# Performance work log

Measured on AMD Instinct MI355X. Metric: run time of the kernel, lower is better.

The kernel has to match this reference:

```python
import jax, jax.numpy as jnp
import numpy as np

N_NODES = 100000
N_EDGES = 1600000
F_IN = 128
HID = 64
HORIZON = 100
NUM_TARGETS = 3


def setup_inputs() -> dict:
    key = jax.random.key(0)
    ks = jax.random.split(key, 7)
    x = jax.random.normal(ks[0], (N_NODES, F_IN), dtype=jnp.float32)
    edge_index = jax.random.randint(ks[1], (2, N_EDGES), 0, N_NODES, dtype=jnp.int64)
    s = 1.0 / np.sqrt(F_IN)
    W_l = jax.random.uniform(ks[2], (HID, F_IN), jnp.float32, -s, s)
    b_l = jax.random.uniform(ks[3], (HID,), jnp.float32, -s, s)
    W_r = jax.random.uniform(ks[4], (HID, F_IN), jnp.float32, -s, s)
    s2 = 1.0 / np.sqrt(HID)
    W_out = jax.random.uniform(ks[5], (NUM_TARGETS * HORIZON, HID), jnp.float32, -s2, s2)
    b_out = jax.random.uniform(ks[6], (NUM_TARGETS * HORIZON,), jnp.float32, -s2, s2)
    return {"x": x, "edge_index": edge_index, "W_l": W_l, "b_l": b_l,
            "W_r": W_r, "W_out": W_out, "b_out": b_out}


def reference(x, edge_index, W_l, b_l, W_r, W_out, b_out):
    n = x.shape[0]
    src, dst = edge_index[0], edge_index[1]
    # gather neighbor features and mean-aggregate per destination node
    msgs = x[src]  # [E, F_IN]
    agg = jax.ops.segment_sum(msgs, dst, num_segments=n)  # [N, F_IN]
    cnt = jax.ops.segment_sum(jnp.ones((edge_index.shape[1],), x.dtype), dst, num_segments=n)
    mean = agg / jnp.maximum(cnt, 1.0)[:, None]
    # SAGEConv: lin_l(aggregated) + lin_r(root), bias only on lin_l
    h = jnp.einsum('nf,hf->nh', mean, W_l) + b_l + jnp.einsum('nf,hf->nh', x, W_r)
    h = jax.nn.relu(h)
    out = jnp.einsum('nh,oh->no', h, W_out) + b_out  # [N, NUM_TARGETS*HORIZON]
    return out.reshape(-1, HORIZON)
```

## Files before the change

kernel.cpp:

```cpp
#include <hip/hip_runtime.h>

#define N_NODES 100000
#define F_IN 128
#define HID 64
#define OUT_F 300
#define WO_ROWS 320
#define NBKT 782
#define ECAP 2688
#define PART_BLOCKS 256
#define GEMM_BLOCKS 391
#define SORT_CAP 6400
#define HS 72

typedef short bf8 __attribute__((ext_vector_type(8)));
typedef float f32x4 __attribute__((ext_vector_type(4)));

__device__ inline unsigned short f2bf(float f) {
    unsigned u = __builtin_bit_cast(unsigned, f);
    u += 0x7fff + ((u >> 16) & 1);
    return (unsigned short)(u >> 16);
}
__device__ inline float b2f(unsigned short h) {
    return __builtin_bit_cast(float, (unsigned)h << 16);
}

__global__ void k_prep(const float* __restrict__ Wl, const float* __restrict__ Wr,
                       const float* __restrict__ Wout,
                       unsigned short* __restrict__ Wc, unsigned short* __restrict__ Wo,
                       int* __restrict__ gcur) {
    int idx = blockIdx.x * blockDim.x + threadIdx.x;
    if (idx < 128 * 128) {
        int c = idx >> 7, k = idx & 127;
        float v = (c < HID) ? Wl[c * F_IN + k] : Wr[(c - HID) * F_IN + k];
        Wc[idx] = f2bf(v);
    } else if (idx < 128 * 128 + WO_ROWS * HID) {
        int j = idx - 128 * 128;
        int o = j >> 6, k = j & 63;
        Wo[j] = (o < OUT_F) ? f2bf(Wout[o * HID + k]) : (unsigned short)0;
    } else {
        int b = idx - 128 * 128 - WO_ROWS * HID;
        if (b < NBKT) gcur[b] = 0;
    }
}

__global__ __launch_bounds__(512) void k_pg(const int* __restrict__ ei,
                                            int* __restrict__ gcur,
                                            unsigned* __restrict__ pedges, int nE,
                                            const float* __restrict__ x,
                                            const unsigned short* __restrict__ Wc,
                                            unsigned short* __restrict__ yz) {
    if (blockIdx.x < PART_BLOCKS) {
        __shared__ unsigned sorted[SORT_CAP];
        __shared__ int hcnt[1024], hoff[1024], hcur[1024];
        __shared__ int wpre[8];
        const int tid = threadIdx.x, lane = tid & 63, wid = tid >> 6;
        const int per = (nE + PART_BLOCKS - 1) / PART_BLOCKS;
        const int e0 = blockIdx.x * per;
        const int e1 = min(e0 + per, nE);
        for (int cb = e0; cb < e1; cb += SORT_CAP) {
            const int cnt = min(SORT_CAP, e1 - cb);
            hcnt[tid * 2] = 0; hcnt[tid * 2 + 1] = 0;
            __syncthreads();
            for (int i = tid; i < cnt; i += 512)
                atomicAdd(&hcnt[ei[nE + cb + i] >> 7], 1);
            __syncthreads();
            int c0 = hcnt[tid * 2], c1 = hcnt[tid * 2 + 1];
            int tsum = c0 + c1;
            int s = tsum;
#pragma unroll
            for (int d = 1; d < 64; d <<= 1) { int t = __shfl_up(s, d, 64); if (lane >= d) s += t; }
            if (lane == 63) wpre[wid] = s;
            __syncthreads();
            if (tid == 0) { int run = 0; for (int w = 0; w < 8; ++w) { int t = wpre[w]; wpre[w] = run; run += t; } }
            __syncthreads();
            int excl = wpre[wid] + (s - tsum);
            hoff[tid * 2 + 0] = excl;       hcur[tid * 2 + 0] = excl;
            hoff[tid * 2 + 1] = excl + c0;  hcur[tid * 2 + 1] = excl + c0;
            __syncthreads();
            for (int i = tid; i < cnt; i += 512) {
                int src = ei[cb + i];
                int dst = ei[nE + cb + i];
                unsigned pk = ((unsigned)src << 7) | (unsigned)(dst & 127);
                int p = atomicAdd(&hcur[dst >> 7], 1);
                sorted[p] = pk;
            }
            __syncthreads();
            for (int b = tid; b < NBKT; b += 512) {
                int c = hcnt[b];
                if (c > 0) {
                    int gp = atomicAdd(&gcur[b], c);
                    unsigned* dst = pedges + (size_t)b * ECAP + gp;
                    int off = hoff[b];
                    for (int i = 0; i < c; ++i) dst[i] = sorted[off + i];
                }
            }
            __syncthreads();
        }
    } else {
        const int wv = threadIdx.x >> 6;
        const int nb = (blockIdx.x - PART_BLOCKS) * 256 + wv * 32;
        if (nb >= N_NODES) return;
        const int lane = threadIdx.x & 63;
        const int lm = lane & 15, lk = lane >> 4;

        f32x4 acc[2][8];
#pragma unroll
        for (int a = 0; a < 2; ++a)
#pragma unroll
            for (int b = 0; b < 8; ++b) acc[a][b] = f32x4{0.f, 0.f, 0.f, 0.f};

#pragma unroll
        for (int kt = 0; kt < 4; ++kt) {
            const int ko = kt * 32 + lk * 8;
            bf8 af[2], bw[8];
#pragma unroll
            for (int mt = 0; mt < 2; ++mt) {
                int row = nb + mt * 16 + lm;
                if (row >= N_NODES) row = N_NODES - 1;
                const float* xp = x + (size_t)row * F_IN + ko;
                float4 v0 = *(const float4*)xp;
                float4 v1 = *(const float4*)(xp + 4);
                bf8 t;
                t[0] = (short)f2bf(v0.x); t[1] = (short)f2bf(v0.y);
                t[2] = (short)f2bf(v0.z); t[3] = (short)f2bf(v0.w);
                t[4] = (short)f2bf(v1.x); t[5] = (short)f2bf(v1.y);
                t[6] = (short)f2bf(v1.z); t[7] = (short)f2bf(v1.w);
                af[mt] = t;
            }
#pragma unroll
            for (int nt = 0; nt < 8; ++nt)
                bw[nt] = *reinterpret_cast<const bf8*>(Wc + (nt * 16 + lm) * 128 + ko);
#pragma unroll
            for (int mt = 0; mt < 2; ++mt)
#pragma unroll
                for (int nt = 0; nt < 8; ++nt)
                    acc[mt][nt] = __builtin_amdgcn_mfma_f32_16x16x32_bf16(af[mt], bw[nt], acc[mt][nt], 0, 0, 0);
        }
#pragma unroll
        for (int mt = 0; mt < 2; ++mt)
#pragma unroll
            for (int r = 0; r < 4; ++r) {
                int node = nb + mt * 16 + lk * 4 + r;
                if (node < N_NODES) {
#pragma unroll
                    for (int nt = 0; nt < 8; ++nt)
                        yz[(size_t)node * 128 + nt * 16 + lm] = f2bf(acc[mt][nt][r]);
                }
            }
    }
}

__global__ __launch_bounds__(512) void k_aggout(const unsigned short* __restrict__ yz,
                                                const unsigned* __restrict__ pedges,
                                                const int* __restrict__ gcur,
                                                const float* __restrict__ bl,
                                                const unsigned short* __restrict__ Wo,
                                                const float* __restrict__ bout,
                                                float* __restrict__ out) {
    __shared__ unsigned esrc[ECAP];
    __shared__ int hcnt[128], hoff[128], hcur[128];
    __shared__ __align__(16) unsigned short h_lds[128 * HS];
    const int tid = threadIdx.x, lane = tid & 63, wv = tid >> 6;
    const int bkt = blockIdx.x;
    int cnt = gcur[bkt]; if (cnt > ECAP) cnt = ECAP;
    const size_t base = (size_t)bkt * ECAP;
    if (tid < 128) hcnt[tid] = 0;
    __syncthreads();
    for (int i = tid; i < cnt; i += 512)
        atomicAdd(&hcnt[pedges[base + i] & 127], 1);
    __syncthreads();
    if (tid < 64) {
        int a = hcnt[2 * tid], b = hcnt[2 * tid + 1];
        int s = a + b;
#pragma unroll
        for (int d = 1; d < 64; d <<= 1) { int t = __shfl_up(s, d, 64); if (lane >= d) s += t; }
        int ex = s - (a + b);
        hoff[2 * tid] = ex;     hcur[2 * tid] = ex;
        hoff[2 * tid + 1] = ex + a; hcur[2 * tid + 1] = ex + a;
    }
    __syncthreads();
    for (int i = tid; i < cnt; i += 512) {
        unsigned e = pedges[base + i];
        int p = atomicAdd(&hcur[e & 127], 1);
        esrc[p] = e >> 7;
    }
    __syncthreads();
    const int q = lane >> 4;
    const int f4 = (lane & 15) * 4;
    float4 blv = *(const float4*)(bl + f4);
    for (int loc = wv; loc < 128; loc += 8) {
        int node = bkt * 128 + loc;
        if (node >= N_NODES) break;
        int st = hoff[loc], dg = hcnt[loc];
        float s0 = 0.f, s1 = 0.f, s2 = 0.f, s3 = 0.f;
        int j = 0;
        for (; j + 8 <= dg; j += 8) {
            unsigned eA = esrc[st + j + q];
            unsigned eB = esrc[st + j + 4 + q];
            uint2 uA = *(const uint2*)(yz + (size_t)eA * 128 + f4);
            uint2 uB = *(const uint2*)(yz + (size_t)eB * 128 + f4);
            s0 += b2f(uA.x & 0xffff) + b2f(uB.x & 0xffff);
            s1 += b2f(uA.x >> 16)    + b2f(uB.x >> 16);
            s2 += b2f(uA.y & 0xffff) + b2f(uB.y & 0xffff);
            s3 += b2f(uA.y >> 16)    + b2f(uB.y >> 16);
        }
        if (j + 4 <= dg) {
            unsigned eA = esrc[st + j + q];
            uint2 uA = *(const uint2*)(yz + (size_t)eA * 128 + f4);
            s0 += b2f(uA.x & 0xffff);
            s1 += b2f(uA.x >> 16);
            s2 += b2f(uA.y & 0xffff);
            s3 += b2f(uA.y >> 16);
            j += 4;
        }
        int rem = dg - j;
        if (q < rem) {
            unsigned eA = esrc[st + j + q];
            uint2 uA = *(const uint2*)(yz + (size_t)eA * 128 + f4);
            s0 += b2f(uA.x & 0xffff);
            s1 += b2f(uA.x >> 16);
            s2 += b2f(uA.y & 0xffff);
            s3 += b2f(uA.y >> 16);
        }
        s0 += __shfl_xor(s0, 16); s0 += __shfl_xor(s0, 32);
        s1 += __shfl_xor(s1, 16); s1 += __shfl_xor(s1, 32);
        s2 += __shfl_xor(s2, 16); s2 += __shfl_xor(s2, 32);
        s3 += __shfl_xor(s3, 16); s3 += __shfl_xor(s3, 32);
        if (q == 0) {
            float inv = 1.0f / fmaxf((float)dg, 1.0f);
            uint2 zu = *(const uint2*)(yz + (size_t)node * 128 + HID + f4);
            float v0 = s0 * inv + b2f(zu.x & 0xffff) + blv.x;
            float v1 = s1 * inv + b2f(zu.x >> 16)    + blv.y;
            float v2 = s2 * inv + b2f(zu.y & 0xffff) + blv.z;
            float v3 = s3 * inv + b2f(zu.y >> 16)    + blv.w;
            uint2 hv;
            hv.x = (unsigned)f2bf(fmaxf(v0, 0.f)) | ((unsigned)f2bf(fmaxf(v1, 0.f)) << 16);
            hv.y = (unsigned)f2bf(fmaxf(v2, 0.f)) | ((unsigned)f2bf(fmaxf(v3, 0.f)) << 16);
            *(uint2*)(h_lds + loc * HS + f4) = hv;
        }
    }
    __syncthreads();
    const int lm = lane & 15, lk = lane >> 4;
    const int nodeL = wv * 16 + lm;
    const int node_g = bkt * 128 + nodeL;
    bf8 ah[2];
#pragma unroll
    for (int k2 = 0; k2 < 2; ++k2)
        ah[k2] = *reinterpret_cast<const bf8*>(h_lds + nodeL * HS + k2 * 32 + lk * 8);

    for (int g = 0; g < 5; ++g) {
        f32x4 acc2[4];
#pragma unroll
        for (int b = 0; b < 4; ++b) acc2[b] = f32x4{0.f, 0.f, 0.f, 0.f};
#pragma unroll
        for (int k2 = 0; k2 < 2; ++k2) {
            bf8 bw[4];
#pragma unroll
            for (int nt = 0; nt < 4; ++nt)
                bw[nt] = *reinterpret_cast<const bf8*>(
                    Wo + (size_t)((g * 4 + nt) * 16 + lm) * HID + k2 * 32 + lk * 8);
#pragma unroll
            for (int nt = 0; nt < 4; ++nt)
                acc2[nt] = __builtin_amdgcn_mfma_f32_16x16x32_bf16(bw[nt], ah[k2], acc2[nt], 0, 0, 0);
        }
#pragma unroll
        for (int nt = 0; nt < 4; ++nt) {
            int ob = (g * 4 + nt) * 16 + lk * 4;
            if (ob + 3 < OUT_F && node_g < N_NODES) {
                float4 bo = *(const float4*)(bout + ob);
                float4 v;
                v.x = acc2[nt][0] + bo.x;
                v.y = acc2[nt][1] + bo.y;
                v.z = acc2[nt][2] + bo.z;
                v.w = acc2[nt][3] + bo.w;
                *(float4*)(out + (size_t)node_g * OUT_F + ob) = v;
            }
        }
    }
}

extern "C" void kernel_launch(void* const* d_in, const int* in_sizes, int n_in,
                              void* d_out, int out_size, void* d_ws, size_t ws_size,
                              hipStream_t stream) {
    const float* x    = (const float*)d_in[0];
    const int*   ei   = (const int*)d_in[1];
    const float* Wl   = (const float*)d_in[2];
    const float* bl   = (const float*)d_in[3];
    const float* Wr   = (const float*)d_in[4];
    const float* Wout = (const float*)d_in[5];
    const float* bout = (const float*)d_in[6];
    float* out = (float*)d_out;

    int nE = in_sizes[1] / 2;

    unsigned short* yz = (unsigned short*)d_ws;
    unsigned* pedges = (unsigned*)(yz + (size_t)N_NODES * 128);
    int* gcur  = (int*)(pedges + (size_t)NBKT * ECAP);
    unsigned short* Wc = (unsigned short*)(gcur + NBKT);
    unsigned short* Wo = Wc + 128 * 128;

    int prep_n = 128 * 128 + WO_ROWS * HID + NBKT;
    k_prep<<<(prep_n + 255) / 256, 256, 0, stream>>>(Wl, Wr, Wout, Wc, Wo, gcur);
    k_pg<<<PART_BLOCKS + GEMM_BLOCKS, 512, 0, stream>>>(ei, gcur, pedges, nE, x, Wc, yz);
    k_aggout<<<NBKT, 512, 0, stream>>>(yz, pedges, gcur, bl, Wo, bout, out);
}
```

Baseline: 142.5 us.

## Split aggregation and output GEMM into separate kernels, interleave two nodes per wave

The fused aggregate+output kernel is split in two. The first kernel gathers neighbours for two destination nodes per wave at once, which raises memory-level parallelism, and writes h to global memory in bf16. The second kernel, with smaller blocks, runs the output MFMA GEMM from global h. This adds a kernel launch and an extra round trip of h through global memory. In return, the gather and the GEMM phases no longer serialize inside one block. The output-store bound check also changes.

```diff
diff --git a/kernel.cpp b/kernel.cpp
--- a/kernel.cpp
+++ b/kernel.cpp
@@ -10,7 +10,6 @@
 #define PART_BLOCKS 256
 #define GEMM_BLOCKS 391
 #define SORT_CAP 6400
-#define HS 72
 
 typedef short bf8 __attribute__((ext_vector_type(8)));
 typedef float f32x4 __attribute__((ext_vector_type(4)));
@@ -150,16 +149,17 @@
     }
 }
 
-__global__ __launch_bounds__(512) void k_aggout(const unsigned short* __restrict__ yz,
-                                                const unsigned* __restrict__ pedges,
-                                                const int* __restrict__ gcur,
-                                                const float* __restrict__ bl,
-                                                const unsigned short* __restrict__ Wo,
-                                                const float* __restrict__ bout,
-                                                float* __restrict__ out) {
+#define LOAD4(e) (*(const uint2*)(yz + (size_t)(e) * 128 + f4))
+#define ACC(sv0, sv1, sv2, sv3, u) \
+    sv0 += b2f(u.x & 0xffff); sv1 += b2f(u.x >> 16); \
+    sv2 += b2f(u.y & 0xffff); sv3 += b2f(u.y >> 16);
+__global__ __launch_bounds__(512) void k_agg3(const unsigned short* __restrict__ yz,
+                                              const unsigned* __restrict__ pedges,
+                                              const int* __restrict__ gcur,
+                                              const float* __restrict__ bl,
+                                              unsigned short* __restrict__ h) {
     __shared__ unsigned esrc[ECAP];
     __shared__ int hcnt[128], hoff[128], hcur[128];
-    __shared__ __align__(16) unsigned short h_lds[128 * HS];
     const int tid = threadIdx.x, lane = tid & 63, wv = tid >> 6;
     const int bkt = blockIdx.x;
     int cnt = gcur[bkt]; if (cnt > ECAP) cnt = ECAP;
@@ -188,65 +188,105 @@
     const int q = lane >> 4;
     const int f4 = (lane & 15) * 4;
     float4 blv = *(const float4*)(bl + f4);
-    for (int loc = wv; loc < 128; loc += 8) {
-        int node = bkt * 128 + loc;
-        if (node >= N_NODES) break;
-        int st = hoff[loc], dg = hcnt[loc];
-        float s0 = 0.f, s1 = 0.f, s2 = 0.f, s3 = 0.f;
-        int j = 0;
-        for (; j + 8 <= dg; j += 8) {
-            unsigned eA = esrc[st + j + q];
-            unsigned eB = esrc[st + j + 4 + q];
-            uint2 uA = *(const uint2*)(yz + (size_t)eA * 128 + f4);
-            uint2 uB = *(const uint2*)(yz + (size_t)eB * 128 + f4);
-            s0 += b2f(uA.x & 0xffff) + b2f(uB.x & 0xffff);
-            s1 += b2f(uA.x >> 16)    + b2f(uB.x >> 16);
-            s2 += b2f(uA.y & 0xffff) + b2f(uB.y & 0xffff);
-            s3 += b2f(uA.y >> 16)    + b2f(uB.y >> 16);
-        }
-        if (j + 4 <= dg) {
-            unsigned eA = esrc[st + j + q];
-            uint2 uA = *(const uint2*)(yz + (size_t)eA * 128 + f4);
-            s0 += b2f(uA.x & 0xffff);
-            s1 += b2f(uA.x >> 16);
-            s2 += b2f(uA.y & 0xffff);
-            s3 += b2f(uA.y >> 16);
-            j += 4;
-        }
-        int rem = dg - j;
-        if (q < rem) {
-            unsigned eA = esrc[st + j + q];
-            uint2 uA = *(const uint2*)(yz + (size_t)eA * 128 + f4);
-            s0 += b2f(uA.x & 0xffff);
-            s1 += b2f(uA.x >> 16);
-            s2 += b2f(uA.y & 0xffff);
-            s3 += b2f(uA.y >> 16);
-        }
-        s0 += __shfl_xor(s0, 16); s0 += __shfl_xor(s0, 32);
-        s1 += __shfl_xor(s1, 16); s1 += __shfl_xor(s1, 32);
-        s2 += __shfl_xor(s2, 16); s2 += __shfl_xor(s2, 32);
-        s3 += __shfl_xor(s3, 16); s3 += __shfl_xor(s3, 32);
+    for (int lp = 0; lp < 8; ++lp) {
+        const int locA = wv * 16 + 2 * lp, locB = locA + 1;
+        const int nodeA = bkt * 128 + locA, nodeB = nodeA + 1;
+        const int stA = hoff[locA], dgA = hcnt[locA];
+        const int stB = hoff[locB], dgB = hcnt[locB];
+        float a0 = 0.f, a1 = 0.f, a2 = 0.f, a3 = 0.f;
+        float b0 = 0.f, b1 = 0.f, b2 = 0.f, b3 = 0.f;
+        int jA = 0, jB = 0;
+        while (jA + 8 <= dgA && jB + 8 <= dgB) {
+            unsigned eA0 = esrc[stA + jA + q],  eA1 = esrc[stA + jA + 4 + q];
+            unsigned eB0 = esrc[stB + jB + q],  eB1 = esrc[stB + jB + 4 + q];
+            uint2 uA0 = LOAD4(eA0), uA1 = LOAD4(eA1);
+            uint2 uB0 = LOAD4(eB0), uB1 = LOAD4(eB1);
+            ACC(a0, a1, a2, a3, uA0) ACC(a0, a1, a2, a3, uA1)
+            ACC(b0, b1, b2, b3, uB0) ACC(b0, b1, b2, b3, uB1)
+            jA += 8; jB += 8;
+        }
+        while (jA + 8 <= dgA) {
+            unsigned eA0 = esrc[stA + jA + q], eA1 = esrc[stA + jA + 4 + q];
+            uint2 uA0 = LOAD4(eA0), uA1 = LOAD4(eA1);
+            ACC(a0, a1, a2, a3, uA0) ACC(a0, a1, a2, a3, uA1)
+            jA += 8;
+        }
+        while (jB + 8 <= dgB) {
+            unsigned eB0 = esrc[stB + jB + q], eB1 = esrc[stB + jB + 4 + q];
+            uint2 uB0 = LOAD4(eB0), uB1 = LOAD4(eB1);
+            ACC(b0, b1, b2, b3, uB0) ACC(b0, b1, b2, b3, uB1)
+            jB += 8;
+        }
+        if (jA + 4 <= dgA) {
+            uint2 u = LOAD4(esrc[stA + jA + q]);
+            ACC(a0, a1, a2, a3, u)
+            jA += 4;
+        }
+        if (jB + 4 <= dgB) {
+            uint2 u = LOAD4(esrc[stB + jB + q]);
+            ACC(b0, b1, b2, b3, u)
+            jB += 4;
+        }
+        if (q < dgA - jA) {
+            uint2 u = LOAD4(esrc[stA + jA + q]);
+            ACC(a0, a1, a2, a3, u)
+        }
+        if (q < dgB - jB) {
+            uint2 u = LOAD4(esrc[stB + jB + q]);
+            ACC(b0, b1, b2, b3, u)
+        }
+        a0 += __shfl_xor(a0, 16); a0 += __shfl_xor(a0, 32);
+        a1 += __shfl_xor(a1, 16); a1 += __shfl_xor(a1, 32);
+        a2 += __shfl_xor(a2, 16); a2 += __shfl_xor(a2, 32);
+        a3 += __shfl_xor(a3, 16); a3 += __shfl_xor(a3, 32);
+        b0 += __shfl_xor(b0, 16); b0 += __shfl_xor(b0, 32);
+        b1 += __shfl_xor(b1, 16); b1 += __shfl_xor(b1, 32);
+        b2 += __shfl_xor(b2, 16); b2 += __shfl_xor(b2, 32);
+        b3 += __shfl_xor(b3, 16); b3 += __shfl_xor(b3, 32);
         if (q == 0) {
-            float inv = 1.0f / fmaxf((float)dg, 1.0f);
-            uint2 zu = *(const uint2*)(yz + (size_t)node * 128 + HID + f4);
-            float v0 = s0 * inv + b2f(zu.x & 0xffff) + blv.x;
-            float v1 = s1 * inv + b2f(zu.x >> 16)    + blv.y;
-            float v2 = s2 * inv + b2f(zu.y & 0xffff) + blv.z;
-            float v3 = s3 * inv + b2f(zu.y >> 16)    + blv.w;
-            uint2 hv;
-            hv.x = (unsigned)f2bf(fmaxf(v0, 0.f)) | ((unsigned)f2bf(fmaxf(v1, 0.f)) << 16);
-            hv.y = (unsigned)f2bf(fmaxf(v2, 0.f)) | ((unsigned)f2bf(fmaxf(v3, 0.f)) << 16);
-            *(uint2*)(h_lds + loc * HS + f4) = hv;
-        }
-    }
-    __syncthreads();
+            if (nodeA < N_NODES) {
+                float inv = 1.0f / fmaxf((float)dgA, 1.0f);
+                uint2 zu = *(const uint2*)(yz + (size_t)nodeA * 128 + HID + f4);
+                float v0 = a0 * inv + b2f(zu.x & 0xffff) + blv.x;
+                float v1 = a1 * inv + b2f(zu.x >> 16)    + blv.y;
+                float v2 = a2 * inv + b2f(zu.y & 0xffff) + blv.z;
+                float v3 = a3 * inv + b2f(zu.y >> 16)    + blv.w;
+                uint2 hv;
+                hv.x = (unsigned)f2bf(fmaxf(v0, 0.f)) | ((unsigned)f2bf(fmaxf(v1, 0.f)) << 16);
+                hv.y = (unsigned)f2bf(fmaxf(v2, 0.f)) | ((unsigned)f2bf(fmaxf(v3, 0.f)) << 16);
+                *(uint2*)(h + (size_t)nodeA * HID + f4) = hv;
+            }
+            if (nodeB < N_NODES) {
+                float inv = 1.0f / fmaxf((float)dgB, 1.0f);
+                uint2 zu = *(const uint2*)(yz + (size_t)nodeB * 128 + HID + f4);
+                float v0 = b0 * inv + b2f(zu.x & 0xffff) + blv.x;
+                float v1 = b1 * inv + b2f(zu.x >> 16)    + blv.y;
+                float v2 = b2 * inv + b2f(zu.y & 0xffff) + blv.z;
+                float v3 = b3 * inv + b2f(zu.y >> 16)    + blv.w;
+                uint2 hv;
+                hv.x = (unsigned)f2bf(fmaxf(v0, 0.f)) | ((unsigned)f2bf(fmaxf(v1, 0.f)) << 16);
+                hv.y = (unsigned)f2bf(fmaxf(v2, 0.f)) | ((unsigned)f2bf(fmaxf(v3, 0.f)) << 16);
+                *(uint2*)(h + (size_t)nodeB * HID + f4) = hv;
+            }
+        }
+    }
+}
+
+__global__ __launch_bounds__(256) void k_fused3(
+    const unsigned short* __restrict__ h, const unsigned short* __restrict__ Wo,
+    const float* __restrict__ bout, float* __restrict__ out) {
+
+    const int tid = threadIdx.x;
+    const int lane = tid & 63;
+    const int wv = tid >> 6;
     const int lm = lane & 15, lk = lane >> 4;
-    const int nodeL = wv * 16 + lm;
-    const int node_g = bkt * 128 + nodeL;
+    const int node_g = blockIdx.x * 64 + wv * 16 + lm;
+    int row = (node_g < N_NODES) ? node_g : (N_NODES - 1);
+
     bf8 ah[2];
 #pragma unroll
     for (int k2 = 0; k2 < 2; ++k2)
-        ah[k2] = *reinterpret_cast<const bf8*>(h_lds + nodeL * HS + k2 * 32 + lk * 8);
+        ah[k2] = *reinterpret_cast<const bf8*>(h + (size_t)row * HID + k2 * 32 + lk * 8);
 
     for (int g = 0; g < 5; ++g) {
         f32x4 acc2[4];
@@ -266,7 +306,7 @@
 #pragma unroll
         for (int nt = 0; nt < 4; ++nt) {
             int ob = (g * 4 + nt) * 16 + lk * 4;
-            if (ob + 3 < OUT_F && node_g < N_NODES) {
+            if (ob < OUT_F && node_g < N_NODES) {
                 float4 bo = *(const float4*)(bout + ob);
                 float4 v;
                 v.x = acc2[nt][0] + bo.x;
@@ -294,7 +334,8 @@
     int nE = in_sizes[1] / 2;
 
     unsigned short* yz = (unsigned short*)d_ws;
-    unsigned* pedges = (unsigned*)(yz + (size_t)N_NODES * 128);
+    unsigned short* h  = yz + (size_t)N_NODES * 128;
+    unsigned* pedges = (unsigned*)(h + (size_t)N_NODES * HID);
     int* gcur  = (int*)(pedges + (size_t)NBKT * ECAP);
     unsigned short* Wc = (unsigned short*)(gcur + NBKT);
     unsigned short* Wo = Wc + 128 * 128;
@@ -302,5 +343,6 @@
     int prep_n = 128 * 128 + WO_ROWS * HID + NBKT;
     k_prep<<<(prep_n + 255) / 256, 256, 0, stream>>>(Wl, Wr, Wout, Wc, Wo, gcur);
     k_pg<<<PART_BLOCKS + GEMM_BLOCKS, 512, 0, stream>>>(ei, gcur, pedges, nE, x, Wc, yz);
-    k_aggout<<<NBKT, 512, 0, stream>>>(yz, pedges, gcur, bl, Wo, bout, out);
-}
+    k_agg3<<<NBKT, 512, 0, stream>>>(yz, pedges, gcur, bl, h);
+    k_fused3<<<(N_NODES + 63) / 64, 256, 0, stream>>>(h, Wo, bout, out);
+}
```

Measured after the change: 141.7 us. About the same (-0.5%).
